# Performance work log

Measured on AMD Instinct MI355X. Metric: run time of the kernel, lower is better.

The kernel has to match this reference:

```python
import jax, jax.numpy as jnp
import numpy as np

NUM_HEADS = 4

def setup_inputs() -> dict:
    key = jax.random.key(0)
    ks = jax.random.split(key, 5)
    B, N, C = 2, 4096, 256
    s = 0.02
    return {
        "x": jax.random.normal(ks[0], (B, N, C), dtype=jnp.float32),
        "qkv_w": jax.random.normal(ks[1], (3 * C, C), dtype=jnp.float32) * s,
        "qkv_b": jax.random.normal(ks[2], (3 * C,), dtype=jnp.float32) * s,
        "out_w": jax.random.normal(ks[3], (C, C), dtype=jnp.float32) * s,
        "out_b": jax.random.normal(ks[4], (C,), dtype=jnp.float32) * s,
    }

def reference(x, qkv_w, qkv_b, out_w, out_b):
    # x: [B, N, C]; manual multi-head self-attention (eval mode, dropout off)
    B, N, C = x.shape
    H = NUM_HEADS
    D = C // H
    qkv = x @ qkv_w.T + qkv_b                      # [B, N, 3C]
    qkv = qkv.reshape(B, N, 3, H, D)
    qkv = jnp.transpose(qkv, (2, 0, 3, 1, 4))      # [3, B, H, N, D]
    q, k, v = qkv[0], qkv[1], qkv[2]
    scale = D ** -0.5
    attn = jnp.einsum('bhnd,bhmd->bhnm', q, k) * scale  # [B, H, N, N]
    attn = jax.nn.softmax(attn, axis=-1)
    out = jnp.einsum('bhnm,bhmd->bhnd', attn, v)   # [B, H, N, D]
    out = jnp.transpose(out, (0, 2, 1, 3)).reshape(B, N, C)
    return out @ out_w.T + out_b
```

## Files before the change

kernel.cpp:

```cpp
#include <hip/hip_runtime.h>

typedef __bf16 bf16x8 __attribute__((ext_vector_type(8)));
typedef float f32x4 __attribute__((ext_vector_type(4)));

#define MFMA_BF16(a, b, c) __builtin_amdgcn_mfma_f32_16x16x32_bf16((a), (b), (c), 0, 0, 0)

#define C1 0.18033688f

static __device__ __forceinline__ unsigned short f2bf(float f) {
    unsigned int u = __float_as_uint(f);
    unsigned int r = (u + 0x7fffu + ((u >> 16) & 1u)) >> 16;
    return (unsigned short)r;
}
static __device__ __forceinline__ float bf2f(unsigned short us) {
    return __uint_as_float(((unsigned int)us) << 16);
}
static __device__ __forceinline__ float exp2_hw(float x) {
    float r;
    asm("v_exp_f32 %0, %1" : "=v"(r) : "v"(x));
    return r;
}
static __device__ __forceinline__ unsigned pack_rh(float a, float b) {
    return __byte_perm(__float_as_uint(a) + 0x8000u, __float_as_uint(b) + 0x8000u, 0x7632);
}
static __device__ __forceinline__ void gload16(const void* g, void* l) {
    __builtin_amdgcn_global_load_lds(
        (const __attribute__((address_space(1))) unsigned int*)g,
        (__attribute__((address_space(3))) unsigned int*)l, 16, 0, 0);
}

static __device__ __forceinline__ void conv_seg8(const void* src, unsigned short* dst, int n,
                                                 int lb, bool f32) {
    const int base = lb * 2048 + (int)threadIdx.x * 8;
    if (base < n) {
        if (f32) {
            const float4 u0 = *(const float4*)((const float*)src + base);
            const float4 u1 = *(const float4*)((const float*)src + base + 4);
            uint4 p;
            p.x = pack_rh(u0.x, u0.y);
            p.y = pack_rh(u0.z, u0.w);
            p.z = pack_rh(u1.x, u1.y);
            p.w = pack_rh(u1.z, u1.w);
            *(uint4*)(dst + base) = p;
        } else {
            *(uint4*)(dst + base) = *(const uint4*)((const unsigned short*)src + base);
        }
    }
}

__global__ __launch_bounds__(256) void convert_kernel(
    const void* __restrict__ x, const void* __restrict__ qw, const void* __restrict__ qb,
    const void* __restrict__ ow, const void* __restrict__ ob,
    unsigned short* __restrict__ xb, unsigned short* __restrict__ qwb,
    unsigned short* __restrict__ qbb, unsigned short* __restrict__ owb,
    unsigned short* __restrict__ obb, int* __restrict__ flag) {
    __shared__ int tot;
    if (threadIdx.x == 0) tot = 0;
    __syncthreads();
    {
        unsigned short v = ((const unsigned short*)x)[threadIdx.x];
        int e = (v >> 7) & 0xFF;
        if (e >= 195) atomicAdd(&tot, 1);
    }
    __syncthreads();
    const bool f32 = (tot >= 8);
    if (blockIdx.x == 0 && threadIdx.x == 0) flag[0] = f32 ? 1 : 0;

    const int bid = blockIdx.x;
    if (bid < 1024)       conv_seg8(x,  xb,  2097152, bid,        f32);
    else if (bid < 1120)  conv_seg8(qw, qwb, 196608,  bid - 1024, f32);
    else if (bid < 1121)  conv_seg8(qb, qbb, 768,     bid - 1120, f32);
    else if (bid < 1153)  conv_seg8(ow, owb, 65536,   bid - 1121, f32);
    else                  conv_seg8(ob, obb, 256,     bid - 1153, f32);
}

template <bool QKV>
__global__ __launch_bounds__(256) void gemm_kernel(
    const unsigned short* __restrict__ A, const unsigned short* __restrict__ W,
    const unsigned short* __restrict__ bias, unsigned short* __restrict__ Cb,
    float* __restrict__ Cf, const int* __restrict__ flag,
    unsigned short* __restrict__ Vt, int Nout) {
    constexpr int K = 256;
    __shared__ __align__(16) char sm[16384];

    const int tid = threadIdx.x;
    const int lane = tid & 63;
    const int wv = tid >> 6;
    const int m16 = lane & 15;
    const int quad = lane >> 4;
    const int bm = blockIdx.x * 64;
    const int bn = blockIdx.y * 64;

    int bgo[2], blo[2];
#pragma unroll
    for (int i = 0; i < 2; i++) {
        const int c = wv * 128 + i * 64 + lane;
        const int r = c >> 3, g = (c & 7) ^ (r & 7);
        bgo[i] = r * (K * 2) + g * 16;
        blo[i] = c * 16;
    }
    int bro[4][2];
#pragma unroll
    for (int t = 0; t < 4; t++)
#pragma unroll
        for (int ks = 0; ks < 2; ks++) {
            const int row = t * 16 + m16;
            bro[t][ks] = row * 64 + ((4 * ks + quad) ^ (m16 & 7)) * 8;
        }

    const char* bg = (const char*)(W + (size_t)bn * K);
    const unsigned short* ap = A + (size_t)(bm + wv * 16 + m16) * K + quad * 8;

#pragma unroll
    for (int i = 0; i < 2; i++) gload16(bg + bgo[i], sm + blo[i]);
    bf16x8 a0 = *(const bf16x8*)(ap);
    bf16x8 a1 = *(const bf16x8*)(ap + 32);

    f32x4 acc[4] = {};
#pragma unroll
    for (int kb = 0; kb < 4; kb++) {
        __syncthreads();
        const int cur = kb & 1;
        bf16x8 a0n, a1n;
        if (kb < 3) {
            bg += 128;
            char* Bdst = sm + (cur ^ 1) * 8192;
#pragma unroll
            for (int i = 0; i < 2; i++) gload16(bg + bgo[i], Bdst + blo[i]);
            a0n = *(const bf16x8*)(ap + (kb + 1) * 64);
            a1n = *(const bf16x8*)(ap + (kb + 1) * 64 + 32);
        }
        const unsigned short* Blds = (const unsigned short*)(sm + cur * 8192);
#pragma unroll
        for (int ks = 0; ks < 2; ks++) {
            const bf16x8 a = ks ? a1 : a0;
#pragma unroll
            for (int t = 0; t < 4; t++) {
                const bf16x8 b = *(const bf16x8*)(Blds + bro[t][ks]);
                acc[t] = MFMA_BF16(a, b, acc[t]);
            }
        }
        if (kb < 3) {
            a0 = a0n;
            a1 = a1n;
        }
    }

    if (QKV && bn >= 512) {
        __syncthreads();
        unsigned short* tr = (unsigned short*)sm;
        const int lr = wv * 16 + quad * 4;
#pragma unroll
        for (int t = 0; t < 4; t++) {
            const float bv = bf2f(bias[bn + t * 16 + m16]);
            uint2 w;
            w.x = pack_rh(acc[t][0] + bv, acc[t][1] + bv);
            w.y = pack_rh(acc[t][2] + bv, acc[t][3] + bv);
            *(uint2*)&tr[(t * 16 + m16) * 72 + lr] = w;
        }
        __syncthreads();
        const int d = tid >> 2;
        const int ch = (tid & 3) * 16;
        const uint4 o4a = *(const uint4*)&tr[d * 72 + ch];
        const uint4 o4b = *(const uint4*)&tr[d * 72 + ch + 8];
        const int hh = (bn - 512) >> 6;
        const int bb = bm >> 12, n0 = bm & 4095;
        unsigned short* vdst = &Vt[((size_t)((bb * 4 + hh) * 64 + d)) * 4096 + n0 + ch];
        *(uint4*)(vdst) = o4a;
        *(uint4*)(vdst + 8) = o4b;
        return;
    }

    const bool outf = (!QKV) && (flag != nullptr) && (*flag != 0);
    const int row0 = bm + wv * 16 + quad * 4;
#pragma unroll
    for (int t = 0; t < 4; t++) {
        const int col = bn + t * 16 + m16;
        const float bv = bf2f(bias[col]);
        float v[4];
#pragma unroll
        for (int r = 0; r < 4; r++) v[r] = acc[t][r] + bv;
        if (QKV) {
            const float sc = (col < 256) ? C1 : 1.0f;
#pragma unroll
            for (int r = 0; r < 4; r++)
                Cb[(size_t)(row0 + r) * 768 + col] = f2bf(v[r] * sc);
        } else {
            if (outf) {
#pragma unroll
                for (int r = 0; r < 4; r++) Cf[(size_t)(row0 + r) * Nout + col] = v[r];
            } else {
#pragma unroll
                for (int r = 0; r < 4; r++) Cb[(size_t)(row0 + r) * Nout + col] = f2bf(v[r]);
            }
        }
    }
}

__global__ __launch_bounds__(256) void attn_kernel(
    const unsigned short* __restrict__ qkv, const unsigned short* __restrict__ Vt,
    unsigned short* __restrict__ attn, int iters) {
    const int N = 4096, C3 = 768;
    __shared__ __align__(16) char sm[65536];

    const int tid = threadIdx.x;
    const int lane = tid & 63;
    const int wv = tid >> 6;
    const int m16 = lane & 15;
    const int quad = lane >> 4;

    const int bh = blockIdx.x & 7;
    const int qt = blockIdx.x >> 3;
    const int b = bh >> 2, h = bh & 3;

    bf16x8 qf[4][2];
#pragma unroll
    for (int j = 0; j < 4; j++)
#pragma unroll
        for (int ks = 0; ks < 2; ks++)
            qf[j][ks] = *(const bf16x8*)(qkv + ((size_t)b * N + qt * 64 + j * 16 + m16) * C3 +
                                         h * 64 + ks * 32 + quad * 8);

    uint4 ones_u;
    ones_u.x = ones_u.y = ones_u.z = ones_u.w = 0x3F803F80u;
    const bf16x8 ones = *(const bf16x8*)&ones_u;

    int kgo[4], vgo[4], klo[4], vlo[4];
#pragma unroll
    for (int i = 0; i < 4; i++) {
        const int c = wv * 256 + i * 64 + lane;
        const int r = c >> 3, g = (c & 7) ^ (r & 7);
        kgo[i] = r * 1536 + g * 16;
        klo[i] = c * 16;
        const int d = c >> 4, gg = (c & 15) ^ (d & 15);
        vgo[i] = d * 8192 + gg * 16;
        vlo[i] = c * 16;
    }
    int kro[2][2], vro[4], pwo[2][4], pro[4];
#pragma unroll
    for (int mb = 0; mb < 2; mb++)
#pragma unroll
        for (int ks = 0; ks < 2; ks++) {
            const int row = wv * 32 + mb * 16 + m16;
            kro[mb][ks] = row * 64 + ((4 * ks + quad) ^ (m16 & 7)) * 8;
        }
#pragma unroll
    for (int t = 0; t < 4; t++) vro[t] = (t * 16 + m16) * 128 + ((wv * 4 + quad) ^ m16) * 8;
#pragma unroll
    for (int mb = 0; mb < 2; mb++)
#pragma unroll
        for (int j = 0; j < 4; j++)
            pwo[mb][j] = wv * 2048 + (j * 16 + m16) * 32 +
                         ((2 * mb + (quad >> 1)) ^ (m16 & 3)) * 8 + (quad & 1) * 4;
#pragma unroll
    for (int j = 0; j < 4; j++)
        pro[j] = wv * 2048 + (j * 16 + m16) * 32 + (quad ^ (m16 & 3)) * 8;

    const char* kgp = (const char*)(qkv + (size_t)b * N * C3 + 256 + h * 64);
    const char* vgp = (const char*)(Vt + (size_t)bh * 64 * N);

#pragma unroll
    for (int i = 0; i < 4; i++) {
        gload16(kgp + kgo[i], sm + klo[i]);
        gload16(vgp + vgo[i], sm + 32768 + vlo[i]);
    }

    f32x4 o[4][4] = {};
    f32x4 o1[4] = {};

    for (int kt = 0; kt < iters; ++kt) {
        __syncthreads();
        const int cur = kt & 1;
        if (kt + 1 < iters) {
            kgp += 128 * 1536;
            vgp += 256;
            char* Kdst = sm + (cur ^ 1) * 16384;
            char* Vdst = sm + 32768 + (cur ^ 1) * 16384;
#pragma unroll
            for (int i = 0; i < 4; i++) {
                gload16(kgp + kgo[i], Kdst + klo[i]);
                gload16(vgp + vgo[i], Vdst + vlo[i]);
            }
        }
        unsigned short* Kb = (unsigned short*)(sm + cur * 16384);
        const unsigned short* Vb = (const unsigned short*)(sm + 32768 + cur * 16384);

        f32x4 s[2][4] = {};
#pragma unroll
        for (int mb = 0; mb < 2; mb++)
#pragma unroll
            for (int ks = 0; ks < 2; ks++) {
                const bf16x8 ka = *(const bf16x8*)(Kb + kro[mb][ks]);
#pragma unroll
                for (int j = 0; j < 4; j++) s[mb][j] = MFMA_BF16(ka, qf[j][ks], s[mb][j]);
            }

#pragma unroll
        for (int mb = 0; mb < 2; mb++)
#pragma unroll
            for (int j = 0; j < 4; j++) {
                const float p0 = exp2_hw(s[mb][j][0]);
                const float p1 = exp2_hw(s[mb][j][1]);
                const float p2 = exp2_hw(s[mb][j][2]);
                const float p3 = exp2_hw(s[mb][j][3]);
                uint2 w;
                w.x = pack_rh(p0, p1);
                w.y = pack_rh(p2, p3);
                *(uint2*)(Kb + pwo[mb][j]) = w;
            }
        asm volatile("s_waitcnt lgkmcnt(0)" ::: "memory");

        bf16x8 pa[4];
#pragma unroll
        for (int j = 0; j < 4; j++) pa[j] = *(const bf16x8*)(Kb + pro[j]);
#pragma unroll
        for (int j = 0; j < 4; j++) o1[j] = MFMA_BF16(pa[j], ones, o1[j]);
#pragma unroll
        for (int t = 0; t < 4; t++) {
            const bf16x8 vb = *(const bf16x8*)(Vb + vro[t]);
#pragma unroll
            for (int j = 0; j < 4; j++) o[j][t] = MFMA_BF16(pa[j], vb, o[j][t]);
        }
    }

    __syncthreads();
    float* Ored = (float*)sm;
    float* lsum = (float*)(sm + 16384);
    if (m16 == 0) {
#pragma unroll
        for (int j = 0; j < 4; j++)
#pragma unroll
            for (int r = 0; r < 4; r++)
                lsum[wv * 64 + j * 16 + quad * 4 + r] = o1[j][r];
    }
    const int row = tid >> 4;
    const int col = (tid & 15) * 4;
#pragma unroll
    for (int j = 0; j < 4; j++) {
#pragma unroll
        for (int t = 0; t < 4; t++)
#pragma unroll
            for (int r = 0; r < 4; r++)
                Ored[(wv * 16 + quad * 4 + r) * 64 + t * 16 + m16] = o[j][t][r];
        __syncthreads();
        f32x4 sum = *(f32x4*)&Ored[row * 64 + col];
        sum += *(f32x4*)&Ored[1024 + row * 64 + col];
        sum += *(f32x4*)&Ored[2048 + row * 64 + col];
        sum += *(f32x4*)&Ored[3072 + row * 64 + col];
        const float lq = lsum[j * 16 + row] + lsum[64 + j * 16 + row] +
                         lsum[128 + j * 16 + row] + lsum[192 + j * 16 + row];
        const int n = qt * 64 + j * 16 + row;
        const float inv = 1.0f / lq;
        uint2 w;
        w.x = pack_rh(sum[0] * inv, sum[1] * inv);
        w.y = pack_rh(sum[2] * inv, sum[3] * inv);
        *(uint2*)&attn[((size_t)b * N + n) * 256 + h * 64 + col] = w;
        __syncthreads();
    }
}

extern "C" void kernel_launch(void* const* d_in, const int* in_sizes, int n_in,
                              void* d_out, int out_size, void* d_ws, size_t ws_size,
                              hipStream_t stream) {
    const int B = 2, N = 4096, H = 4;
    const int M = B * N;

    char* wsb = (char*)d_ws;
    int* flag = (int*)wsb;
    unsigned short* xb      = (unsigned short*)(wsb + 64);
    unsigned short* qwb     = xb + 2097152;
    unsigned short* qbb     = qwb + 196608;
    unsigned short* owb     = qbb + 768;
    unsigned short* obb     = owb + 65536;
    unsigned short* qkv_ws  = obb + 256;
    unsigned short* Vt_ws   = qkv_ws + 6291456;
    unsigned short* attn_ws = Vt_ws + 2097152;

    convert_kernel<<<1154, 256, 0, stream>>>(d_in[0], d_in[1], d_in[2], d_in[3], d_in[4],
                                             xb, qwb, qbb, owb, obb, flag);

    gemm_kernel<true><<<dim3(M / 64, 768 / 64), 256, 0, stream>>>(
        xb, qwb, qbb, qkv_ws, nullptr, nullptr, Vt_ws, 768);

    attn_kernel<<<512, 256, 0, stream>>>(qkv_ws, Vt_ws, attn_ws, 32);

    gemm_kernel<false><<<dim3(M / 64, 256 / 64), 256, 0, stream>>>(
        attn_ws, owb, obb, (unsigned short*)d_out, (float*)d_out, flag, nullptr, 256);
}
```

Baseline: 144.8 us.

## Give each wave private K/V LDS tiles with register-staged prefetch, dropping block barriers

```diff
diff --git a/kernel.cpp b/kernel.cpp
--- a/kernel.cpp
+++ b/kernel.cpp
@@ -197,7 +197,7 @@
     }
 }
 
-__global__ __launch_bounds__(256) void attn_kernel(
+__global__ __launch_bounds__(256, 2) void attn_kernel(
     const unsigned short* __restrict__ qkv, const unsigned short* __restrict__ Vt,
     unsigned short* __restrict__ attn, int iters) {
     const int N = 4096, C3 = 768;
@@ -213,6 +213,8 @@
     const int qt = blockIdx.x >> 3;
     const int b = bh >> 2, h = bh & 3;
 
+    char* wbase = sm + wv * 16384;
+
     bf16x8 qf[4][2];
 #pragma unroll
     for (int j = 0; j < 4; j++)
@@ -225,65 +227,64 @@
     ones_u.x = ones_u.y = ones_u.z = ones_u.w = 0x3F803F80u;
     const bf16x8 ones = *(const bf16x8*)&ones_u;
 
-    int kgo[4], vgo[4], klo[4], vlo[4];
+    int kgo[4], klo[4], vgo[4], vlo[4];
 #pragma unroll
     for (int i = 0; i < 4; i++) {
-        const int c = wv * 256 + i * 64 + lane;
-        const int r = c >> 3, g = (c & 7) ^ (r & 7);
+        const int c = i * 64 + lane;
+        const int r = c >> 3, g = c & 7;
         kgo[i] = r * 1536 + g * 16;
-        klo[i] = c * 16;
-        const int d = c >> 4, gg = (c & 15) ^ (d & 15);
-        vgo[i] = d * 8192 + gg * 16;
-        vlo[i] = c * 16;
+        klo[i] = r * 128 + (g ^ (r & 7)) * 16;
+        const int d = c >> 2, lc = c & 3;
+        vgo[i] = d * 8192 + lc * 16;
+        vlo[i] = d * 64 + (lc ^ (d & 3)) * 16;
     }
     int kro[2][2], vro[4], pwo[2][4], pro[4];
 #pragma unroll
     for (int mb = 0; mb < 2; mb++)
 #pragma unroll
-        for (int ks = 0; ks < 2; ks++) {
-            const int row = wv * 32 + mb * 16 + m16;
-            kro[mb][ks] = row * 64 + ((4 * ks + quad) ^ (m16 & 7)) * 8;
-        }
-#pragma unroll
-    for (int t = 0; t < 4; t++) vro[t] = (t * 16 + m16) * 128 + ((wv * 4 + quad) ^ m16) * 8;
+        for (int ks = 0; ks < 2; ks++)
+            kro[mb][ks] = (mb * 16 + m16) * 64 + ((4 * ks + quad) ^ (m16 & 7)) * 8;
+#pragma unroll
+    for (int t = 0; t < 4; t++) vro[t] = (t * 16 + m16) * 32 + (quad ^ (m16 & 3)) * 8;
 #pragma unroll
     for (int mb = 0; mb < 2; mb++)
 #pragma unroll
         for (int j = 0; j < 4; j++)
-            pwo[mb][j] = wv * 2048 + (j * 16 + m16) * 32 +
+            pwo[mb][j] = (j * 16 + m16) * 32 +
                          ((2 * mb + (quad >> 1)) ^ (m16 & 3)) * 8 + (quad & 1) * 4;
 #pragma unroll
     for (int j = 0; j < 4; j++)
-        pro[j] = wv * 2048 + (j * 16 + m16) * 32 + (quad ^ (m16 & 3)) * 8;
-
-    const char* kgp = (const char*)(qkv + (size_t)b * N * C3 + 256 + h * 64);
-    const char* vgp = (const char*)(Vt + (size_t)bh * 64 * N);
-
+        pro[j] = (j * 16 + m16) * 32 + (quad ^ (m16 & 3)) * 8;
+
+    const char* kgp = (const char*)(qkv + ((size_t)b * N + wv * 32) * C3 + 256 + h * 64);
+    const char* vgp = (const char*)(Vt + (size_t)bh * 64 * N) + wv * 64;
+
+    uint4 kr[4], vr[4];
 #pragma unroll
     for (int i = 0; i < 4; i++) {
-        gload16(kgp + kgo[i], sm + klo[i]);
-        gload16(vgp + vgo[i], sm + 32768 + vlo[i]);
+        kr[i] = *(const uint4*)(kgp + kgo[i]);
+        vr[i] = *(const uint4*)(vgp + vgo[i]);
+    }
+#pragma unroll
+    for (int i = 0; i < 4; i++) {
+        *(uint4*)(wbase + klo[i]) = kr[i];
+        *(uint4*)(wbase + 8192 + vlo[i]) = vr[i];
+    }
+    kgp += 128 * 1536;
+    vgp += 256;
+#pragma unroll
+    for (int i = 0; i < 4; i++) {
+        kr[i] = *(const uint4*)(kgp + kgo[i]);
+        vr[i] = *(const uint4*)(vgp + vgo[i]);
     }
 
     f32x4 o[4][4] = {};
     f32x4 o1[4] = {};
 
     for (int kt = 0; kt < iters; ++kt) {
-        __syncthreads();
         const int cur = kt & 1;
-        if (kt + 1 < iters) {
-            kgp += 128 * 1536;
-            vgp += 256;
-            char* Kdst = sm + (cur ^ 1) * 16384;
-            char* Vdst = sm + 32768 + (cur ^ 1) * 16384;
-#pragma unroll
-            for (int i = 0; i < 4; i++) {
-                gload16(kgp + kgo[i], Kdst + klo[i]);
-                gload16(vgp + vgo[i], Vdst + vlo[i]);
-            }
-        }
-        unsigned short* Kb = (unsigned short*)(sm + cur * 16384);
-        const unsigned short* Vb = (const unsigned short*)(sm + 32768 + cur * 16384);
+        unsigned short* Kb = (unsigned short*)(wbase + cur * 4096);
+        const unsigned short* Vb = (const unsigned short*)(wbase + 8192 + cur * 4096);
 
         f32x4 s[2][4] = {};
 #pragma unroll
@@ -294,6 +295,16 @@
 #pragma unroll
                 for (int j = 0; j < 4; j++) s[mb][j] = MFMA_BF16(ka, qf[j][ks], s[mb][j]);
             }
+
+        if (kt + 1 < iters) {
+            char* Ko = wbase + (cur ^ 1) * 4096;
+            char* Vo = wbase + 8192 + (cur ^ 1) * 4096;
+#pragma unroll
+            for (int i = 0; i < 4; i++) {
+                *(uint4*)(Ko + klo[i]) = kr[i];
+                *(uint4*)(Vo + vlo[i]) = vr[i];
+            }
+        }
 
 #pragma unroll
         for (int mb = 0; mb < 2; mb++)
@@ -320,6 +331,16 @@
             const bf16x8 vb = *(const bf16x8*)(Vb + vro[t]);
 #pragma unroll
             for (int j = 0; j < 4; j++) o[j][t] = MFMA_BF16(pa[j], vb, o[j][t]);
+        }
+
+        if (kt + 2 < iters) {
+            kgp += 128 * 1536;
+            vgp += 256;
+#pragma unroll
+            for (int i = 0; i < 4; i++) {
+                kr[i] = *(const uint4*)(kgp + kgo[i]);
+                vr[i] = *(const uint4*)(vgp + vgo[i]);
+            }
         }
     }
 
```

Measured after the change: 184.4 us. +27.4%, slower.
